# Optimization experiments

Measured on AMD Instinct MI355X. Metric: run time of the kernel, lower is better.

## Reference

```python
import jax, jax.numpy as jnp
import numpy as np

LEAK = 0.01  # torch LeakyReLU default negative_slope

def lrelu(x):
    return jnp.where(x >= 0, x, LEAK * x)

def edge_conv(x, src, dst, ea, W1, b1, W2, b2):
    # message: cat(x_i=target, x_j=source, edge_attr) -> Linear -> LeakyReLU -> Linear
    m = jnp.concatenate([x[dst], x[src], ea], axis=1)          # [E, 2F+Fe]
    h = lrelu(m @ W1 + b1) @ W2 + b2                            # [E, H]
    n = x.shape[0]
    agg = jnp.full((n, h.shape[1]), jnp.inf, h.dtype).at[dst].min(h)  # scatter-min at target
    return jnp.where(jnp.isfinite(agg), agg, jnp.zeros_like(agg))     # empty nodes -> 0


def setup_inputs() -> dict:
    key = jax.random.key(0)
    ks = jax.random.split(key, 20)
    B, N, E = 4, 20000, 640000
    NF, AD, EF, H = 2, 1, 1, 8
    inp = {
        "node_features": jax.random.randint(ks[0], (B, N, NF), 0, 10, dtype=jnp.int32),
        "actions": jax.random.normal(ks[1], (B, N), dtype=jnp.float32),
        "edge_index": jax.random.randint(ks[2], (B, 2, E), 0, N, dtype=jnp.int64),
        "edge_features": jax.random.normal(ks[3], (B, E, EF), dtype=jnp.float32),
    }
    d0 = NF + AD  # 3
    def lin(k, fin, fout):
        s = 1.0 / np.sqrt(fin)
        k1, k2 = jax.random.split(k)
        return (jax.random.uniform(k1, (fin, fout), jnp.float32, -s, s),
                jax.random.uniform(k2, (fout,), jnp.float32, -s, s))
    inp["c1_W1"], inp["c1_b1"] = lin(ks[4], 2 * d0 + EF, H)
    inp["c1_W2"], inp["c1_b2"] = lin(ks[5], H, H)
    inp["c2_W1"], inp["c2_b1"] = lin(ks[6], 2 * H + 1, H)
    inp["c2_W2"], inp["c2_b2"] = lin(ks[7], H, H)
    inp["c3_W1"], inp["c3_b1"] = lin(ks[8], 2 * H + 1, H)
    inp["c3_W2"], inp["c3_b2"] = lin(ks[9], H, H)
    inp["lin_W"], inp["lin_b"] = lin(ks[10], d0 + H, 1)
    return inp


def reference(node_features, actions, edge_index, edge_features,
              c1_W1, c1_b1, c1_W2, c1_b2,
              c2_W1, c2_b1, c2_W2, c2_b2,
              c3_W1, c3_b1, c3_W2, c3_b2,
              lin_W, lin_b):
    # x = int(node_features) concat actions  -> float
    x0 = jnp.concatenate([node_features.astype(jnp.int32).astype(jnp.float32),
                          actions[..., None]], axis=-1)  # [B,N,3]

    def per_graph(x0g, eig, eag):
        src, dst = eig[0], eig[1]  # flow source_to_target: x_j=src, x_i=dst
        h = lrelu(edge_conv(x0g, src, dst, eag, c1_W1, c1_b1, c1_W2, c1_b2))
        h = lrelu(edge_conv(h, src, dst, eag, c2_W1, c2_b1, c2_W2, c2_b2))
        h = lrelu(edge_conv(h, src, dst, eag, c3_W1, c3_b1, c3_W2, c3_b2))
        xc = jnp.concatenate([x0g, h], axis=1)  # [N, 3+8]
        return jnp.sum(xc, axis=0)              # sum-pool over nodes

    pooled = jax.vmap(per_graph)(x0, edge_index, edge_features)  # [B, 11]
    return pooled @ lin_W + lin_b  # [B, 1]
```

## Files before the change

### kernel.cpp

```cpp
#include <hip/hip_runtime.h>
#include <hip/hip_cooperative_groups.h>

namespace cg = cooperative_groups;

#define LEAK 0.01f
#define BS 128
#define PCHUNK 4096
#define PT 512
#define CT 512
#define MAXNB 256
#define CPGMAX 256

__device__ __forceinline__ float lrelu(float v) {
    return v >= 0.f ? v : LEAK * v;
}

__device__ __forceinline__ unsigned int fmin_encode(float x) {
    unsigned int u = __float_as_uint(x);
    return (u & 0x80000000u) ? ~u : (u | 0x80000000u);
}
__device__ __forceinline__ float fmin_decode(unsigned int k) {
    unsigned int u = (k & 0x80000000u) ? (k ^ 0x80000000u) : ~k;
    return __uint_as_float(u);
}

__device__ __forceinline__ unsigned int bf16_rne(float f) {
    unsigned int u = __float_as_uint(f);
    return (u + 0x7FFFu + ((u >> 16) & 1u)) >> 16;
}

__device__ __forceinline__ void block_add(float c, float* dst) {
    __shared__ float wsum[8];
#pragma unroll
    for (int off = 32; off > 0; off >>= 1) c += __shfl_down(c, off, 64);
    int lane = threadIdx.x & 63;
    int wave = threadIdx.x >> 6;
    if (lane == 0) wsum[wave] = c;
    __syncthreads();
    if (threadIdx.x == 0) {
        float s = 0.f;
        int nw = blockDim.x >> 6;
        for (int w = 0; w < nw; ++w) s += wsum[w];
        atomicAdd(dst, s);
    }
}


__device__ void init_body(
    const int* __restrict__ nf, const float* __restrict__ act,
    const float* __restrict__ W1, const float* __restrict__ b1,
    const float* __restrict__ lw, const float* __restrict__ lb,
    float* __restrict__ a1, unsigned short* __restrict__ a2,
    float* __restrict__ out, int N, int b, int ib) {
    int t = threadIdx.x;
    int n = ib * PT + t;
    float c = 0.f;
    if (n < N) {
        size_t i = (size_t)b * N + n;
        float x0 = (float)nf[i * 2 + 0];
        float x1 = (float)nf[i * 2 + 1];
        float x2 = act[i];
        float v1[8], v2[8];
#pragma unroll
        for (int j = 0; j < 8; ++j) {
            v1[j] = b1[j] + x0 * W1[0 * 8 + j] + x1 * W1[1 * 8 + j] + x2 * W1[2 * 8 + j];
            v2[j] =         x0 * W1[3 * 8 + j] + x1 * W1[4 * 8 + j] + x2 * W1[5 * 8 + j];
        }
        float4* o1 = (float4*)(a1 + i * 8);
        o1[0] = make_float4(v1[0], v1[1], v1[2], v1[3]);
        o1[1] = make_float4(v1[4], v1[5], v1[6], v1[7]);
        unsigned int w[4];
#pragma unroll
        for (int q = 0; q < 4; ++q)
            w[q] = bf16_rne(v2[2 * q]) | (bf16_rne(v2[2 * q + 1]) << 16);
        *(int4*)(a2 + i * 8) = make_int4(w[0], w[1], w[2], w[3]);
        c = x0 * lw[0] + x1 * lw[1] + x2 * lw[2];
        if (n == 0) c += lb[0];
    }
    block_add(c, &out[b]);
}

__device__ void part_body(
    const int* __restrict__ ei, const float* __restrict__ ea,
    int2* __restrict__ pairs, int* __restrict__ ofs,
    int E, int NB, int CPG, int b, int c,
    int* __restrict__ lc, int* __restrict__ lofs, int* __restrict__ ts) {
    int t = threadIdx.x;
    for (int i = t; i < NB; i += PT) lc[i] = 0;
    __syncthreads();

    int e0 = c * PCHUNK;
    int end = min(e0 + PCHUNK, E);
    const int* srow = ei + (size_t)b * 2 * E;
    const int* drow = srow + E;

    int pk[PCHUNK / PT];
#pragma unroll
    for (int j = 0; j < PCHUNK / PT; ++j) {
        int e = e0 + j * PT + t;
        int p = -1;
        if (e < end) {
            int d = drow[e];
            int bin = d >> 7;
            int r = atomicAdd(&lc[bin], 1);
            p = bin | ((d & 127) << 10) | (r << 17);
        }
        pk[j] = p;
    }
    __syncthreads();

    int v = (t < NB) ? lc[t] : 0;
    ts[t] = v;
    __syncthreads();
    int incl = v;
    for (int off = 1; off < PT; off <<= 1) {
        int add = (t >= off) ? ts[t - off] : 0;
        __syncthreads();
        incl += add;
        ts[t] = incl;
        __syncthreads();
    }
    if (t < NB) lofs[t] = incl - v;
    if (t == PT - 1) lofs[NB] = incl;
    __syncthreads();

    for (int i = t; i <= NB; i += PT) {
        int w = lofs[i];
        ofs[((size_t)b * (NB + 1) + i) * CPG + c] = w;
        if (i < NB) lc[i] = w;
    }
    __syncthreads();

    size_t pbase = (size_t)b * E + e0;
#pragma unroll
    for (int j = 0; j < PCHUNK / PT; ++j) {
        int e = e0 + j * PT + t;
        if (e < end) {
            int p = pk[j];
            int bin = p & 1023;
            int dl = (p >> 10) & 127;
            int r = p >> 17;
            int pos = lc[bin] + r;
            pairs[pbase + pos] =
                make_int2(srow[e] | (dl << 16), __float_as_int(ea[(size_t)b * E + e]));
        }
    }
}

__device__ __forceinline__ void conv_edge_compute(
    const float* we, const float* bb, const float* __restrict__ W2,
    int2 p, int4 raw, const float* __restrict__ a1s,
    unsigned int* __restrict__ acc) {
    int dl = (p.x >> 16) & 127;
    float eav = __int_as_float(p.y);
    unsigned int wq[4] = {(unsigned int)raw.x, (unsigned int)raw.y,
                          (unsigned int)raw.z, (unsigned int)raw.w};
    float a2v[8];
#pragma unroll
    for (int q = 0; q < 4; ++q) {
        a2v[2 * q]     = __uint_as_float(wq[q] << 16);
        a2v[2 * q + 1] = __uint_as_float(wq[q] & 0xFFFF0000u);
    }
    float h1[8];
#pragma unroll
    for (int j = 0; j < 8; ++j) {
        h1[j] = a1s[dl * 9 + j] + a2v[j];
        h1[j] = fmaf(eav, we[j], h1[j]);
        h1[j] = lrelu(h1[j]);
    }
    float h2[8];
#pragma unroll
    for (int j = 0; j < 8; ++j) h2[j] = bb[j];
#pragma unroll
    for (int kk = 0; kk < 8; ++kk) {
        float hk = h1[kk];
#pragma unroll
        for (int j = 0; j < 8; ++j) h2[j] = fmaf(hk, W2[kk * 8 + j], h2[j]);
    }
#pragma unroll
    for (int j = 0; j < 8; ++j)
        atomicMin(&acc[dl * 9 + j], fmin_encode(h2[j]));
}

__device__ void conv_edges_runs(
    const unsigned short* __restrict__ a2g, const float* we, const float* bb,
    const float* __restrict__ W2, const int2* __restrict__ pairsg,
    const int* __restrict__ ofb, int CPG,
    const float* __restrict__ a1s, unsigned int* __restrict__ acc,
    int* __restrict__ rs, int* __restrict__ re) {
    int t = threadIdx.x;
    for (int c = t; c < CPG; c += CT) {
        rs[c] = ofb[c];
        re[c] = ofb[CPG + c];
    }
    __syncthreads();
    int sw = t >> 5, sub = t & 31;
    const int nsw = CT >> 5;
    for (int c = sw; c < CPG; c += nsw) {
        int cb = c * PCHUNK;
        int k1 = cb + re[c];
        for (int k = cb + rs[c] + sub; k < k1; k += 32) {
            int2 p = pairsg[k];
            int4 v = *(const int4*)(a2g + (size_t)(p.x & 0xFFFF) * 8);
            conv_edge_compute(we, bb, W2, p, v, a1s, acc);
        }
    }
}

__device__ void conv_mid_body(
    const float* __restrict__ a1, const unsigned short* __restrict__ a2,
    const float* __restrict__ w1e, const float* __restrict__ W2,
    const float* __restrict__ b2,
    const float* __restrict__ nW1, const float* __restrict__ nb1,
    const int* __restrict__ ofs, const int2* __restrict__ pairs,
    float* __restrict__ na1, unsigned short* __restrict__ na2,
    int N, int NB, int CPG, int E, int b, int bin,
    float* __restrict__ a1s, unsigned int* __restrict__ acc,
    int* __restrict__ rs, int* __restrict__ re) {
    int n0 = bin << 7;
    int nCnt = min(BS, N - n0);
    int t = threadIdx.x;
    size_t node0 = (size_t)b * N + n0;

    for (int i = t; i < nCnt * 8; i += CT)
        a1s[(i >> 3) * 9 + (i & 7)] = a1[node0 * 8 + i];
    for (int i = t; i < BS * 9; i += CT) acc[i] = 0xFFFFFFFFu;
    float we[8], bb[8];
#pragma unroll
    for (int j = 0; j < 8; ++j) { we[j] = w1e[j]; bb[j] = b2[j]; }
    __syncthreads();

    conv_edges_runs(a2 + (size_t)b * N * 8, we, bb, W2,
                    pairs + (size_t)b * E,
                    ofs + ((size_t)b * (NB + 1) + bin) * CPG,
                    CPG, a1s, acc, rs, re);
    __syncthreads();

    for (int i = t; i < nCnt * 8; i += CT) {
        float v = fmin_decode(acc[(i >> 3) * 9 + (i & 7)]);
        unsigned int u = __float_as_uint(v);
        if ((u & 0x7F800000u) == 0x7F800000u) v = 0.f;
        a1s[(i >> 3) * 9 + (i & 7)] = lrelu(v);
    }
    __syncthreads();

    for (int nh = t; nh < nCnt * 2; nh += CT) {
        int node = nh >> 1, half = nh & 1;
        float h[8];
#pragma unroll
        for (int j = 0; j < 8; ++j) h[j] = a1s[node * 9 + j];
        float v[8];
#pragma unroll
        for (int j = 0; j < 8; ++j) v[j] = half ? 0.f : nb1[j];
        const float* Wbase = nW1 + (half ? 64 : 0);
#pragma unroll
        for (int k = 0; k < 8; ++k) {
            float hk = h[k];
#pragma unroll
            for (int j = 0; j < 8; ++j) v[j] = fmaf(hk, Wbase[k * 8 + j], v[j]);
        }
        if (half) {
            unsigned int w[4];
#pragma unroll
            for (int q = 0; q < 4; ++q)
                w[q] = bf16_rne(v[2 * q]) | (bf16_rne(v[2 * q + 1]) << 16);
            *(int4*)(na2 + (node0 + node) * 8) = make_int4(w[0], w[1], w[2], w[3]);
        } else {
            float4* o = (float4*)(na1 + (node0 + node) * 8);
            o[0] = make_float4(v[0], v[1], v[2], v[3]);
            o[1] = make_float4(v[4], v[5], v[6], v[7]);
        }
    }
    __syncthreads();
}

__device__ void conv_final_body(
    const float* __restrict__ a1, const unsigned short* __restrict__ a2,
    const float* __restrict__ w1e, const float* __restrict__ W2,
    const float* __restrict__ b2, const float* __restrict__ lw,
    const int* __restrict__ ofs, const int2* __restrict__ pairs,
    float* __restrict__ out, int N, int NB, int CPG, int E, int b, int bin,
    float* __restrict__ a1s, unsigned int* __restrict__ acc,
    int* __restrict__ rs, int* __restrict__ re) {
    int n0 = bin << 7;
    int nCnt = min(BS, N - n0);
    int t = threadIdx.x;
    size_t node0 = (size_t)b * N + n0;

    for (int i = t; i < nCnt * 8; i += CT)
        a1s[(i >> 3) * 9 + (i & 7)] = a1[node0 * 8 + i];
    for (int i = t; i < BS * 9; i += CT) acc[i] = 0xFFFFFFFFu;
    float we[8], bb[8];
#pragma unroll
    for (int j = 0; j < 8; ++j) { we[j] = w1e[j]; bb[j] = b2[j]; }
    __syncthreads();

    conv_edges_runs(a2 + (size_t)b * N * 8, we, bb, W2,
                    pairs + (size_t)b * E,
                    ofs + ((size_t)b * (NB + 1) + bin) * CPG,
                    CPG, a1s, acc, rs, re);
    __syncthreads();

    float c = 0.f;
    if (t < nCnt) {
#pragma unroll
        for (int j = 0; j < 8; ++j) {
            float v = fmin_decode(acc[t * 9 + j]);
            unsigned int u = __float_as_uint(v);
            if ((u & 0x7F800000u) == 0x7F800000u) v = 0.f;
            c = fmaf(lrelu(v), lw[3 + j], c);
        }
    }
    __syncthreads();
    block_add(c, &out[b]);
}


struct MegaParams {
    const int* ei; const float* ea;
    int2* pairs; int* ofs;
    const int* nf; const float* act;
    const float* W11; const float* b11; const float* W21; const float* b21;
    const float* W12; const float* b12; const float* W22; const float* b22;
    const float* W13; const float* b13; const float* W23; const float* b23;
    const float* lw; const float* lb;
    float* a1A; unsigned short* a2A; float* a1B; unsigned short* a2B;
    float* out;
    int E, N, NB, CPG, initBlocks;
};

__global__ __launch_bounds__(512, 8) void mega_kernel(MegaParams P) {
    cg::grid_group grid = cg::this_grid();
    __shared__ int lc[MAXNB];
    __shared__ int lofs[MAXNB + 1];
    __shared__ int ts[PT];
    __shared__ float a1s[BS * 9];
    __shared__ unsigned int acc[BS * 9];
    __shared__ int rs[CPGMAX];
    __shared__ int re[CPGMAX];
    int b = blockIdx.y, bx = blockIdx.x;

    if (bx < P.CPG)
        part_body(P.ei, P.ea, P.pairs, P.ofs, P.E, P.NB, P.CPG, b, bx, lc, lofs, ts);
    else if (bx - P.CPG < P.initBlocks)
        init_body(P.nf, P.act, P.W11, P.b11, P.lw, P.lb, P.a1A, P.a2A, P.out,
                  P.N, b, bx - P.CPG);
    __threadfence();
    grid.sync();
    if (bx < P.NB)
        conv_mid_body(P.a1A, P.a2A, P.W11 + 6 * 8, P.W21, P.b21, P.W12, P.b12,
                      P.ofs, P.pairs, P.a1B, P.a2B, P.N, P.NB, P.CPG, P.E,
                      b, bx, a1s, acc, rs, re);
    __threadfence();
    grid.sync();
    if (bx < P.NB)
        conv_mid_body(P.a1B, P.a2B, P.W12 + 16 * 8, P.W22, P.b22, P.W13, P.b13,
                      P.ofs, P.pairs, P.a1A, P.a2A, P.N, P.NB, P.CPG, P.E,
                      b, bx, a1s, acc, rs, re);
    __threadfence();
    grid.sync();
    if (bx < P.NB)
        conv_final_body(P.a1A, P.a2A, P.W13 + 16 * 8, P.W23, P.b23, P.lw,
                        P.ofs, P.pairs, P.out, P.N, P.NB, P.CPG, P.E,
                        b, bx, a1s, acc, rs, re);
}


__global__ __launch_bounds__(PT) void part_init_kernel(
    const int* __restrict__ ei, const float* __restrict__ ea,
    int2* __restrict__ pairs, int* __restrict__ ofs,
    const int* __restrict__ nf, const float* __restrict__ act,
    const float* __restrict__ W1, const float* __restrict__ b1,
    const float* __restrict__ lw, const float* __restrict__ lb,
    float* __restrict__ a1, unsigned short* __restrict__ a2,
    float* __restrict__ out, int E, int N, int NB, int CPG) {
    __shared__ int lc[MAXNB];
    __shared__ int lofs[MAXNB + 1];
    __shared__ int ts[PT];
    int b = blockIdx.y;
    if (blockIdx.x >= CPG) {
        init_body(nf, act, W1, b1, lw, lb, a1, a2, out, N, b, blockIdx.x - CPG);
        return;
    }
    part_body(ei, ea, pairs, ofs, E, NB, CPG, b, blockIdx.x, lc, lofs, ts);
}

__global__ __launch_bounds__(CT) void conv_mid_kernel(
    const float* __restrict__ a1, const unsigned short* __restrict__ a2,
    const float* __restrict__ w1e, const float* __restrict__ W2,
    const float* __restrict__ b2,
    const float* __restrict__ nW1, const float* __restrict__ nb1,
    const int* __restrict__ ofs, const int2* __restrict__ pairs,
    float* __restrict__ na1, unsigned short* __restrict__ na2,
    int N, int NB, int CPG, int E) {
    __shared__ float a1s[BS * 9];
    __shared__ unsigned int acc[BS * 9];
    __shared__ int rs[CPGMAX];
    __shared__ int re[CPGMAX];
    conv_mid_body(a1, a2, w1e, W2, b2, nW1, nb1, ofs, pairs, na1, na2,
                  N, NB, CPG, E, blockIdx.y, blockIdx.x, a1s, acc, rs, re);
}

__global__ __launch_bounds__(CT) void conv_final_kernel(
    const float* __restrict__ a1, const unsigned short* __restrict__ a2,
    const float* __restrict__ w1e, const float* __restrict__ W2,
    const float* __restrict__ b2, const float* __restrict__ lw,
    const int* __restrict__ ofs, const int2* __restrict__ pairs,
    float* __restrict__ out, int N, int NB, int CPG, int E) {
    __shared__ float a1s[BS * 9];
    __shared__ unsigned int acc[BS * 9];
    __shared__ int rs[CPGMAX];
    __shared__ int re[CPGMAX];
    conv_final_body(a1, a2, w1e, W2, b2, lw, ofs, pairs, out,
                    N, NB, CPG, E, blockIdx.y, blockIdx.x, a1s, acc, rs, re);
}


__global__ __launch_bounds__(256) void node_init_kernel(
    const int* __restrict__ nf, const float* __restrict__ act,
    float* __restrict__ x0, int BN) {
    int tid = blockIdx.x * blockDim.x + threadIdx.x;
    if (tid >= BN) return;
    x0[tid * 3 + 0] = (float)nf[tid * 2 + 0];
    x0[tid * 3 + 1] = (float)nf[tid * 2 + 1];
    x0[tid * 3 + 2] = act[tid];
}

template <int D>
__global__ __launch_bounds__(256) void edge_conv_kernel(
    const float* __restrict__ x, const int* __restrict__ ei,
    const float* __restrict__ ea,
    const float* __restrict__ W1, const float* __restrict__ b1,
    const float* __restrict__ W2, const float* __restrict__ b2,
    unsigned int* __restrict__ agg, int E, int N, int B) {
    int tid = blockIdx.x * blockDim.x + threadIdx.x;
    if (tid >= B * E) return;
    int b = tid / E;
    int e = tid - b * E;
    const int* eb = ei + (size_t)b * 2 * E;
    int s = eb[e];
    int d = eb[E + e];
    const float* xi = x + ((size_t)b * N + d) * D;
    const float* xj = x + ((size_t)b * N + s) * D;
    constexpr int M = 2 * D + 1;
    float m[M];
#pragma unroll
    for (int k = 0; k < D; ++k) { m[k] = xi[k]; m[D + k] = xj[k]; }
    m[2 * D] = ea[(size_t)b * E + e];
    float h1[8];
#pragma unroll
    for (int j = 0; j < 8; ++j) h1[j] = b1[j];
#pragma unroll
    for (int k = 0; k < M; ++k) {
        float mk = m[k];
#pragma unroll
        for (int j = 0; j < 8; ++j) h1[j] = fmaf(mk, W1[k * 8 + j], h1[j]);
    }
#pragma unroll
    for (int j = 0; j < 8; ++j) h1[j] = lrelu(h1[j]);
    float h2[8];
#pragma unroll
    for (int j = 0; j < 8; ++j) h2[j] = b2[j];
#pragma unroll
    for (int k = 0; k < 8; ++k) {
        float hk = h1[k];
#pragma unroll
        for (int j = 0; j < 8; ++j) h2[j] = fmaf(hk, W2[k * 8 + j], h2[j]);
    }
    unsigned int* ag = agg + ((size_t)b * N + d) * 8;
#pragma unroll
    for (int j = 0; j < 8; ++j) atomicMin(&ag[j], fmin_encode(h2[j]));
}

__global__ __launch_bounds__(256) void finalize_kernel(
    unsigned int* __restrict__ agg, int total) {
    int tid = blockIdx.x * blockDim.x + threadIdx.x;
    if (tid >= total) return;
    float v = fmin_decode(agg[tid]);
    unsigned int u = __float_as_uint(v);
    if ((u & 0x7F800000u) == 0x7F800000u) v = 0.f;
    ((float*)agg)[tid] = lrelu(v);
}

__global__ __launch_bounds__(256) void pool_kernel(
    const float* __restrict__ x0, const float* __restrict__ h,
    const float* __restrict__ lw, const float* __restrict__ lb,
    float* __restrict__ out, int N) {
    int b = blockIdx.y;
    int n = blockIdx.x * blockDim.x + threadIdx.x;
    float c = 0.f;
    if (n < N) {
        const float* x = x0 + ((size_t)b * N + n) * 3;
        const float* hh = h + ((size_t)b * N + n) * 8;
        c = x[0] * lw[0] + x[1] * lw[1] + x[2] * lw[2];
#pragma unroll
        for (int k = 0; k < 8; ++k) c = fmaf(hh[k], lw[3 + k], c);
        if (n == 0) c += lb[0];
    }
    block_add(c, &out[b]);
}


static inline size_t align256(size_t x) { return (x + 255) & ~(size_t)255; }

extern "C" void kernel_launch(void* const* d_in, const int* in_sizes, int n_in,
                              void* d_out, int out_size, void* d_ws, size_t ws_size,
                              hipStream_t stream) {
    const int B = 4;
    const int N = in_sizes[1] / B;
    const int E = in_sizes[2] / (2 * B);

    const int*   nf  = (const int*)d_in[0];
    const float* act = (const float*)d_in[1];
    const int*   ei  = (const int*)d_in[2];
    const float* ea  = (const float*)d_in[3];
    const float* c1_W1 = (const float*)d_in[4];
    const float* c1_b1 = (const float*)d_in[5];
    const float* c1_W2 = (const float*)d_in[6];
    const float* c1_b2 = (const float*)d_in[7];
    const float* c2_W1 = (const float*)d_in[8];
    const float* c2_b1 = (const float*)d_in[9];
    const float* c2_W2 = (const float*)d_in[10];
    const float* c2_b2 = (const float*)d_in[11];
    const float* c3_W1 = (const float*)d_in[12];
    const float* c3_b1 = (const float*)d_in[13];
    const float* c3_W2 = (const float*)d_in[14];
    const float* c3_b2 = (const float*)d_in[15];
    const float* lw    = (const float*)d_in[16];
    const float* lb    = (const float*)d_in[17];
    float* out = (float*)d_out;

    const int BN = B * N;
    const int BE = B * E;
    const int NB = (N + BS - 1) / BS;
    const int CPG = (E + PCHUNK - 1) / PCHUNK;
    const int initBlocks = (N + PT - 1) / PT;

    char* ws = (char*)d_ws;
    size_t off = 0;
    float* a1A = (float*)(ws + off);           off += align256((size_t)BN * 8 * 4);
    float* a1B = (float*)(ws + off);           off += align256((size_t)BN * 8 * 4);
    unsigned short* a2A = (unsigned short*)(ws + off); off += align256((size_t)BN * 8 * 2);
    unsigned short* a2B = (unsigned short*)(ws + off); off += align256((size_t)BN * 8 * 2);
    int* ofs    = (int*)(ws + off);    off += align256((size_t)B * (NB + 1) * CPG * 4);
    int2* pairs = (int2*)(ws + off);   off += align256((size_t)BE * 8);
    float* x0   = (float*)(ws + off);  off += align256((size_t)BN * 3 * 4);
    const bool useFast = (off <= ws_size) && (NB <= MAXNB) && (CPG <= CPGMAX) &&
                         (N <= 32768);

    hipMemsetAsync(out, 0, (size_t)B * sizeof(float), stream);

    if (useFast) {
        const int gx = (CPG + initBlocks > NB) ? (CPG + initBlocks) : NB;

        int dev = 0;
        hipGetDevice(&dev);
        int numCU = 0;
        hipDeviceGetAttribute(&numCU, hipDeviceAttributeMultiprocessorCount, dev);
        int occ = 0;
        hipOccupancyMaxActiveBlocksPerMultiprocessor(&occ, mega_kernel, 512, 0);
        const bool canCoop = (occ > 0) && ((size_t)occ * (size_t)numCU >=
                                           (size_t)gx * (size_t)B);

        if (canCoop) {
            MegaParams P;
            P.ei = ei; P.ea = ea; P.pairs = pairs; P.ofs = ofs;
            P.nf = nf; P.act = act;
            P.W11 = c1_W1; P.b11 = c1_b1; P.W21 = c1_W2; P.b21 = c1_b2;
            P.W12 = c2_W1; P.b12 = c2_b1; P.W22 = c2_W2; P.b22 = c2_b2;
            P.W13 = c3_W1; P.b13 = c3_b1; P.W23 = c3_W2; P.b23 = c3_b2;
            P.lw = lw; P.lb = lb;
            P.a1A = a1A; P.a2A = a2A; P.a1B = a1B; P.a2B = a2B;
            P.out = out;
            P.E = E; P.N = N; P.NB = NB; P.CPG = CPG; P.initBlocks = initBlocks;
            void* args[] = {&P};
            hipLaunchCooperativeKernel((void*)mega_kernel, dim3(gx, B),
                                       dim3(512), args, 0, stream);
        } else {
            dim3 pgrid(CPG + initBlocks, B);
            dim3 cgrid(NB, B);
            part_init_kernel<<<pgrid, PT, 0, stream>>>(
                ei, ea, pairs, ofs, nf, act, c1_W1, c1_b1, lw, lb,
                a1A, a2A, out, E, N, NB, CPG);
            conv_mid_kernel<<<cgrid, CT, 0, stream>>>(
                a1A, a2A, c1_W1 + 6 * 8, c1_W2, c1_b2, c2_W1, c2_b1,
                ofs, pairs, a1B, a2B, N, NB, CPG, E);
            conv_mid_kernel<<<cgrid, CT, 0, stream>>>(
                a1B, a2B, c2_W1 + 16 * 8, c2_W2, c2_b2, c3_W1, c3_b1,
                ofs, pairs, a1A, a2A, N, NB, CPG, E);
            conv_final_kernel<<<cgrid, CT, 0, stream>>>(
                a1A, a2A, c3_W1 + 16 * 8, c3_W2, c3_b2, lw,
                ofs, pairs, out, N, NB, CPG, E);
        }
    } else {
        const int egrid = (BE + 255) / 256;
        const int aggTotal = BN * 8;
        const int agrid = (aggTotal + 255) / 256;
        const size_t aggBytes = (size_t)aggTotal * 4;
        unsigned int* uA = (unsigned int*)a1A;
        unsigned int* uB = (unsigned int*)a1B;

        node_init_kernel<<<(BN + 255) / 256, 256, 0, stream>>>(nf, act, x0, BN);

        hipMemsetAsync(uA, 0xFF, aggBytes, stream);
        edge_conv_kernel<3><<<egrid, 256, 0, stream>>>(
            x0, ei, ea, c1_W1, c1_b1, c1_W2, c1_b2, uA, E, N, B);
        finalize_kernel<<<agrid, 256, 0, stream>>>(uA, aggTotal);

        hipMemsetAsync(uB, 0xFF, aggBytes, stream);
        edge_conv_kernel<8><<<egrid, 256, 0, stream>>>(
            (const float*)uA, ei, ea, c2_W1, c2_b1, c2_W2, c2_b2, uB, E, N, B);
        finalize_kernel<<<agrid, 256, 0, stream>>>(uB, aggTotal);

        hipMemsetAsync(uA, 0xFF, aggBytes, stream);
        edge_conv_kernel<8><<<egrid, 256, 0, stream>>>(
            (const float*)uB, ei, ea, c3_W1, c3_b1, c3_W2, c3_b2, uA, E, N, B);
        finalize_kernel<<<agrid, 256, 0, stream>>>(uA, aggTotal);

        dim3 plgrid((N + 255) / 256, B);
        pool_kernel<<<plgrid, 256, 0, stream>>>(x0, (const float*)uA, lw, lb, out, N);
    }
}
```

Before: 208.7 us.

## Add per-bin sort by destination node to replace shared atomicMin with register reductions

Adds a sort stage after partitioning that counts edges per bin globally, builds per-destination-node histograms, and scatters edge pairs into a fully destination-sorted array. The three conv stages then give each 32-lane group one destination node, keep running minima in registers and reduce with shuffles, which removes the eight shared-memory atomicMin operations per edge and the float-encoding step. The cost is an extra pass over all edges with a grid-wide sync, a second edge buffer, and load imbalance when node degrees vary.

```diff
diff --git a/kernel.cpp b/kernel.cpp
--- a/kernel.cpp
+++ b/kernel.cpp
@@ -7,7 +7,6 @@
 #define BS 128
 #define PCHUNK 4096
 #define PT 512
-#define CT 512
 #define MAXNB 256
 #define CPGMAX 256
 
@@ -82,7 +81,7 @@
 
 __device__ void part_body(
     const int* __restrict__ ei, const float* __restrict__ ea,
-    int2* __restrict__ pairs, int* __restrict__ ofs,
+    int2* __restrict__ pairs, int* __restrict__ ofs, int* __restrict__ bcnt,
     int E, int NB, int CPG, int b, int c,
     int* __restrict__ lc, int* __restrict__ lofs, int* __restrict__ ts) {
     int t = threadIdx.x;
@@ -110,6 +109,7 @@
     __syncthreads();
 
     int v = (t < NB) ? lc[t] : 0;
+    if (t < NB && v) atomicAdd(&bcnt[b * NB + t], v);
     ts[t] = v;
     __syncthreads();
     int incl = v;
@@ -147,62 +147,131 @@
     }
 }
 
-__device__ __forceinline__ void conv_edge_compute(
-    const float* we, const float* bb, const float* __restrict__ W2,
-    int2 p, int4 raw, const float* __restrict__ a1s,
-    unsigned int* __restrict__ acc) {
-    int dl = (p.x >> 16) & 127;
-    float eav = __int_as_float(p.y);
-    unsigned int wq[4] = {(unsigned int)raw.x, (unsigned int)raw.y,
-                          (unsigned int)raw.z, (unsigned int)raw.w};
-    float a2v[8];
-#pragma unroll
-    for (int q = 0; q < 4; ++q) {
-        a2v[2 * q]     = __uint_as_float(wq[q] << 16);
-        a2v[2 * q + 1] = __uint_as_float(wq[q] & 0xFFFF0000u);
-    }
-    float h1[8];
-#pragma unroll
-    for (int j = 0; j < 8; ++j) {
-        h1[j] = a1s[dl * 9 + j] + a2v[j];
-        h1[j] = fmaf(eav, we[j], h1[j]);
-        h1[j] = lrelu(h1[j]);
-    }
-    float h2[8];
-#pragma unroll
-    for (int j = 0; j < 8; ++j) h2[j] = bb[j];
-#pragma unroll
-    for (int kk = 0; kk < 8; ++kk) {
-        float hk = h1[kk];
-#pragma unroll
-        for (int j = 0; j < 8; ++j) h2[j] = fmaf(hk, W2[kk * 8 + j], h2[j]);
-    }
-#pragma unroll
-    for (int j = 0; j < 8; ++j)
-        atomicMin(&acc[dl * 9 + j], fmin_encode(h2[j]));
-}
-
-__device__ void conv_edges_runs(
-    const unsigned short* __restrict__ a2g, const float* we, const float* bb,
-    const float* __restrict__ W2, const int2* __restrict__ pairsg,
-    const int* __restrict__ ofb, int CPG,
-    const float* __restrict__ a1s, unsigned int* __restrict__ acc,
-    int* __restrict__ rs, int* __restrict__ re) {
+__device__ void sort_body(
+    const int* __restrict__ ofs_bbin, const int* __restrict__ bcnt_b,
+    const int2* __restrict__ pairsg, int2* __restrict__ spairsg,
+    int* __restrict__ segofs_b, int* __restrict__ dlofs_bbin,
+    int NB, int CPG, int bin,
+    int* __restrict__ rs, int* __restrict__ re,
+    int* __restrict__ hist, int* __restrict__ cursor, int* __restrict__ red) {
     int t = threadIdx.x;
-    for (int c = t; c < CPG; c += CT) {
-        rs[c] = ofb[c];
-        re[c] = ofb[CPG + c];
-    }
-    __syncthreads();
+    for (int c = t; c < CPG; c += PT) {
+        rs[c] = ofs_bbin[c];
+        re[c] = ofs_bbin[CPG + c];
+    }
+    for (int i = t; i < BS; i += PT) hist[i] = 0;
+
+    int part = 0;
+    for (int i = t; i < bin; i += PT) part += bcnt_b[i];
+#pragma unroll
+    for (int off = 32; off > 0; off >>= 1) part += __shfl_down(part, off, 64);
+    if ((t & 63) == 0) red[t >> 6] = part;
+    __syncthreads();
+    if (t == 0) {
+        int s = 0;
+        for (int w = 0; w < PT / 64; ++w) s += red[w];
+        red[0] = s;
+    }
+    __syncthreads();
+    int seg0 = red[0];
+    int cnt = bcnt_b[bin];
+    if (t == 0) {
+        segofs_b[bin] = seg0;
+        if (bin == NB - 1) segofs_b[NB] = seg0 + cnt;
+    }
+
     int sw = t >> 5, sub = t & 31;
-    const int nsw = CT >> 5;
+    const int nsw = PT >> 5;
+    for (int c = sw; c < CPG; c += nsw) {
+        int cb = c * PCHUNK;
+        int k1 = cb + re[c];
+        for (int k = cb + rs[c] + sub; k < k1; k += 32)
+            atomicAdd(&hist[(pairsg[k].x >> 16) & 127], 1);
+    }
+    __syncthreads();
+
+    if (t < BS) cursor[t] = hist[t];
+    __syncthreads();
+    for (int off = 1; off < BS; off <<= 1) {
+        int add = 0;
+        if (t < BS && t >= off) add = cursor[t - off];
+        __syncthreads();
+        if (t < BS) cursor[t] += add;
+        __syncthreads();
+    }
+    if (t < BS) cursor[t] -= hist[t];
+    __syncthreads();
+
+    if (t < BS) dlofs_bbin[t] = cursor[t];
+    if (t == 0) dlofs_bbin[BS] = cnt;
+    __syncthreads();
+
     for (int c = sw; c < CPG; c += nsw) {
         int cb = c * PCHUNK;
         int k1 = cb + re[c];
         for (int k = cb + rs[c] + sub; k < k1; k += 32) {
             int2 p = pairsg[k];
-            int4 v = *(const int4*)(a2g + (size_t)(p.x & 0xFFFF) * 8);
-            conv_edge_compute(we, bb, W2, p, v, a1s, acc);
+            int pos = atomicAdd(&cursor[(p.x >> 16) & 127], 1);
+            spairsg[seg0 + pos] = p;
+        }
+    }
+}
+
+__device__ void conv_core_sorted(
+    const unsigned short* __restrict__ a2g, const float* we, const float* bb,
+    const float* __restrict__ W2, const int2* __restrict__ spairsg,
+    int seg0, const int* __restrict__ dlofs,
+    const float* __restrict__ a1s, float* __restrict__ hres) {
+    int t = threadIdx.x;
+    int sw = t >> 5, sub = t & 31;
+    const int nsw = PT >> 5;
+    for (int dl = sw; dl < BS; dl += nsw) {
+        int g0 = seg0 + dlofs[dl];
+        int g1 = seg0 + dlofs[dl + 1];
+        float a1r[8];
+#pragma unroll
+        for (int j = 0; j < 8; ++j) a1r[j] = a1s[dl * 9 + j];
+        float m[8];
+#pragma unroll
+        for (int j = 0; j < 8; ++j) m[j] = __builtin_inff();
+        for (int k = g0 + sub; k < g1; k += 32) {
+            int2 p = spairsg[k];
+            float eav = __int_as_float(p.y);
+            int4 raw = *(const int4*)(a2g + (size_t)(p.x & 0xFFFF) * 8);
+            unsigned int wq[4] = {(unsigned int)raw.x, (unsigned int)raw.y,
+                                  (unsigned int)raw.z, (unsigned int)raw.w};
+            float h1[8];
+#pragma unroll
+            for (int q = 0; q < 4; ++q) {
+                h1[2 * q]     = a1r[2 * q]     + __uint_as_float(wq[q] << 16);
+                h1[2 * q + 1] = a1r[2 * q + 1] + __uint_as_float(wq[q] & 0xFFFF0000u);
+            }
+#pragma unroll
+            for (int j = 0; j < 8; ++j) {
+                h1[j] = fmaf(eav, we[j], h1[j]);
+                h1[j] = lrelu(h1[j]);
+            }
+            float h2[8];
+#pragma unroll
+            for (int j = 0; j < 8; ++j) h2[j] = bb[j];
+#pragma unroll
+            for (int kk = 0; kk < 8; ++kk) {
+                float hk = h1[kk];
+#pragma unroll
+                for (int j = 0; j < 8; ++j) h2[j] = fmaf(hk, W2[kk * 8 + j], h2[j]);
+            }
+#pragma unroll
+            for (int j = 0; j < 8; ++j) m[j] = fminf(m[j], h2[j]);
+        }
+#pragma unroll
+        for (int off = 16; off > 0; off >>= 1) {
+#pragma unroll
+            for (int j = 0; j < 8; ++j)
+                m[j] = fminf(m[j], __shfl_down(m[j], off, 32));
+        }
+        if (sub == 0) {
+#pragma unroll
+            for (int j = 0; j < 8; ++j) hres[dl * 9 + j] = m[j];
         }
     }
 }
@@ -212,39 +281,39 @@
     const float* __restrict__ w1e, const float* __restrict__ W2,
     const float* __restrict__ b2,
     const float* __restrict__ nW1, const float* __restrict__ nb1,
-    const int* __restrict__ ofs, const int2* __restrict__ pairs,
+    const int* __restrict__ segofs, const int* __restrict__ dlofs_g,
+    const int2* __restrict__ spairs,
     float* __restrict__ na1, unsigned short* __restrict__ na2,
-    int N, int NB, int CPG, int E, int b, int bin,
-    float* __restrict__ a1s, unsigned int* __restrict__ acc,
-    int* __restrict__ rs, int* __restrict__ re) {
+    int N, int NB, int E, int b, int bin,
+    float* __restrict__ a1s, float* __restrict__ hres, int* __restrict__ dlo) {
     int n0 = bin << 7;
     int nCnt = min(BS, N - n0);
     int t = threadIdx.x;
     size_t node0 = (size_t)b * N + n0;
 
-    for (int i = t; i < nCnt * 8; i += CT)
+    for (int i = t; i < nCnt * 8; i += PT)
         a1s[(i >> 3) * 9 + (i & 7)] = a1[node0 * 8 + i];
-    for (int i = t; i < BS * 9; i += CT) acc[i] = 0xFFFFFFFFu;
+    const int* dsrc = dlofs_g + ((size_t)b * NB + bin) * (BS + 1);
+    for (int i = t; i <= BS; i += PT) dlo[i] = dsrc[i];
     float we[8], bb[8];
 #pragma unroll
     for (int j = 0; j < 8; ++j) { we[j] = w1e[j]; bb[j] = b2[j]; }
-    __syncthreads();
-
-    conv_edges_runs(a2 + (size_t)b * N * 8, we, bb, W2,
-                    pairs + (size_t)b * E,
-                    ofs + ((size_t)b * (NB + 1) + bin) * CPG,
-                    CPG, a1s, acc, rs, re);
-    __syncthreads();
-
-    for (int i = t; i < nCnt * 8; i += CT) {
-        float v = fmin_decode(acc[(i >> 3) * 9 + (i & 7)]);
+    int seg0 = segofs[(size_t)b * (NB + 1) + bin];
+    __syncthreads();
+
+    conv_core_sorted(a2 + (size_t)b * N * 8, we, bb, W2,
+                     spairs + (size_t)b * E, seg0, dlo, a1s, hres);
+    __syncthreads();
+
+    for (int i = t; i < nCnt * 8; i += PT) {
+        float v = hres[(i >> 3) * 9 + (i & 7)];
         unsigned int u = __float_as_uint(v);
         if ((u & 0x7F800000u) == 0x7F800000u) v = 0.f;
         a1s[(i >> 3) * 9 + (i & 7)] = lrelu(v);
     }
     __syncthreads();
 
-    for (int nh = t; nh < nCnt * 2; nh += CT) {
+    for (int nh = t; nh < nCnt * 2; nh += PT) {
         int node = nh >> 1, half = nh & 1;
         float h[8];
 #pragma unroll
@@ -278,34 +347,34 @@
     const float* __restrict__ a1, const unsigned short* __restrict__ a2,
     const float* __restrict__ w1e, const float* __restrict__ W2,
     const float* __restrict__ b2, const float* __restrict__ lw,
-    const int* __restrict__ ofs, const int2* __restrict__ pairs,
-    float* __restrict__ out, int N, int NB, int CPG, int E, int b, int bin,
-    float* __restrict__ a1s, unsigned int* __restrict__ acc,
-    int* __restrict__ rs, int* __restrict__ re) {
+    const int* __restrict__ segofs, const int* __restrict__ dlofs_g,
+    const int2* __restrict__ spairs,
+    float* __restrict__ out, int N, int NB, int E, int b, int bin,
+    float* __restrict__ a1s, float* __restrict__ hres, int* __restrict__ dlo) {
     int n0 = bin << 7;
     int nCnt = min(BS, N - n0);
     int t = threadIdx.x;
     size_t node0 = (size_t)b * N + n0;
 
-    for (int i = t; i < nCnt * 8; i += CT)
+    for (int i = t; i < nCnt * 8; i += PT)
         a1s[(i >> 3) * 9 + (i & 7)] = a1[node0 * 8 + i];
-    for (int i = t; i < BS * 9; i += CT) acc[i] = 0xFFFFFFFFu;
+    const int* dsrc = dlofs_g + ((size_t)b * NB + bin) * (BS + 1);
+    for (int i = t; i <= BS; i += PT) dlo[i] = dsrc[i];
     float we[8], bb[8];
 #pragma unroll
     for (int j = 0; j < 8; ++j) { we[j] = w1e[j]; bb[j] = b2[j]; }
-    __syncthreads();
-
-    conv_edges_runs(a2 + (size_t)b * N * 8, we, bb, W2,
-                    pairs + (size_t)b * E,
-                    ofs + ((size_t)b * (NB + 1) + bin) * CPG,
-                    CPG, a1s, acc, rs, re);
+    int seg0 = segofs[(size_t)b * (NB + 1) + bin];
+    __syncthreads();
+
+    conv_core_sorted(a2 + (size_t)b * N * 8, we, bb, W2,
+                     spairs + (size_t)b * E, seg0, dlo, a1s, hres);
     __syncthreads();
 
     float c = 0.f;
     if (t < nCnt) {
 #pragma unroll
         for (int j = 0; j < 8; ++j) {
-            float v = fmin_decode(acc[t * 9 + j]);
+            float v = hres[t * 9 + j];
             unsigned int u = __float_as_uint(v);
             if ((u & 0x7F800000u) == 0x7F800000u) v = 0.f;
             c = fmaf(lrelu(v), lw[3 + j], c);
@@ -318,7 +387,7 @@
 
 struct MegaParams {
     const int* ei; const float* ea;
-    int2* pairs; int* ofs;
+    int2* pairs; int2* spairs; int* ofs; int* bcnt; int* segofs; int* dlofs;
     const int* nf; const float* act;
     const float* W11; const float* b11; const float* W21; const float* b21;
     const float* W12; const float* b12; const float* W22; const float* b22;
@@ -335,40 +404,52 @@
     __shared__ int lofs[MAXNB + 1];
     __shared__ int ts[PT];
     __shared__ float a1s[BS * 9];
-    __shared__ unsigned int acc[BS * 9];
-    __shared__ int rs[CPGMAX];
-    __shared__ int re[CPGMAX];
+    __shared__ float hres[BS * 9];
+    __shared__ int dlo[BS + 1];
+    __shared__ int hist[BS];
+    __shared__ int cursor[BS];
+    __shared__ int red[PT / 64];
     int b = blockIdx.y, bx = blockIdx.x;
 
     if (bx < P.CPG)
-        part_body(P.ei, P.ea, P.pairs, P.ofs, P.E, P.NB, P.CPG, b, bx, lc, lofs, ts);
+        part_body(P.ei, P.ea, P.pairs, P.ofs, P.bcnt, P.E, P.NB, P.CPG, b, bx,
+                  lc, lofs, ts);
     else if (bx - P.CPG < P.initBlocks)
         init_body(P.nf, P.act, P.W11, P.b11, P.lw, P.lb, P.a1A, P.a2A, P.out,
                   P.N, b, bx - P.CPG);
     __threadfence();
     grid.sync();
     if (bx < P.NB)
+        sort_body(P.ofs + ((size_t)b * (P.NB + 1) + bx) * P.CPG,
+                  P.bcnt + (size_t)b * P.NB,
+                  P.pairs + (size_t)b * P.E, P.spairs + (size_t)b * P.E,
+                  P.segofs + (size_t)b * (P.NB + 1),
+                  P.dlofs + ((size_t)b * P.NB + bx) * (BS + 1),
+                  P.NB, P.CPG, bx, lc, lofs, hist, cursor, red);
+    __threadfence();
+    grid.sync();
+    if (bx < P.NB)
         conv_mid_body(P.a1A, P.a2A, P.W11 + 6 * 8, P.W21, P.b21, P.W12, P.b12,
-                      P.ofs, P.pairs, P.a1B, P.a2B, P.N, P.NB, P.CPG, P.E,
-                      b, bx, a1s, acc, rs, re);
+                      P.segofs, P.dlofs, P.spairs, P.a1B, P.a2B,
+                      P.N, P.NB, P.E, b, bx, a1s, hres, dlo);
     __threadfence();
     grid.sync();
     if (bx < P.NB)
         conv_mid_body(P.a1B, P.a2B, P.W12 + 16 * 8, P.W22, P.b22, P.W13, P.b13,
-                      P.ofs, P.pairs, P.a1A, P.a2A, P.N, P.NB, P.CPG, P.E,
-                      b, bx, a1s, acc, rs, re);
+                      P.segofs, P.dlofs, P.spairs, P.a1A, P.a2A,
+                      P.N, P.NB, P.E, b, bx, a1s, hres, dlo);
     __threadfence();
     grid.sync();
     if (bx < P.NB)
         conv_final_body(P.a1A, P.a2A, P.W13 + 16 * 8, P.W23, P.b23, P.lw,
-                        P.ofs, P.pairs, P.out, P.N, P.NB, P.CPG, P.E,
-                        b, bx, a1s, acc, rs, re);
+                        P.segofs, P.dlofs, P.spairs, P.out,
+                        P.N, P.NB, P.E, b, bx, a1s, hres, dlo);
 }
 
 
 __global__ __launch_bounds__(PT) void part_init_kernel(
     const int* __restrict__ ei, const float* __restrict__ ea,
-    int2* __restrict__ pairs, int* __restrict__ ofs,
+    int2* __restrict__ pairs, int* __restrict__ ofs, int* __restrict__ bcnt,
     const int* __restrict__ nf, const float* __restrict__ act,
     const float* __restrict__ W1, const float* __restrict__ b1,
     const float* __restrict__ lw, const float* __restrict__ lb,
@@ -382,37 +463,55 @@
         init_body(nf, act, W1, b1, lw, lb, a1, a2, out, N, b, blockIdx.x - CPG);
         return;
     }
-    part_body(ei, ea, pairs, ofs, E, NB, CPG, b, blockIdx.x, lc, lofs, ts);
-}
-
-__global__ __launch_bounds__(CT) void conv_mid_kernel(
+    part_body(ei, ea, pairs, ofs, bcnt, E, NB, CPG, b, blockIdx.x, lc, lofs, ts);
+}
+
+__global__ __launch_bounds__(PT) void sort_kernel(
+    const int* __restrict__ ofs, const int* __restrict__ bcnt,
+    const int2* __restrict__ pairs, int2* __restrict__ spairs,
+    int* __restrict__ segofs, int* __restrict__ dlofs,
+    int NB, int CPG, int E) {
+    __shared__ int rs[CPGMAX];
+    __shared__ int re[CPGMAX];
+    __shared__ int hist[BS];
+    __shared__ int cursor[BS];
+    __shared__ int red[PT / 64];
+    int b = blockIdx.y, bin = blockIdx.x;
+    sort_body(ofs + ((size_t)b * (NB + 1) + bin) * CPG, bcnt + (size_t)b * NB,
+              pairs + (size_t)b * E, spairs + (size_t)b * E,
+              segofs + (size_t)b * (NB + 1),
+              dlofs + ((size_t)b * NB + bin) * (BS + 1),
+              NB, CPG, bin, rs, re, hist, cursor, red);
+}
+
+__global__ __launch_bounds__(PT) void conv_mid_kernel(
     const float* __restrict__ a1, const unsigned short* __restrict__ a2,
     const float* __restrict__ w1e, const float* __restrict__ W2,
     const float* __restrict__ b2,
     const float* __restrict__ nW1, const float* __restrict__ nb1,
-    const int* __restrict__ ofs, const int2* __restrict__ pairs,
+    const int* __restrict__ segofs, const int* __restrict__ dlofs,
+    const int2* __restrict__ spairs,
     float* __restrict__ na1, unsigned short* __restrict__ na2,
-    int N, int NB, int CPG, int E) {
+    int N, int NB, int E) {
     __shared__ float a1s[BS * 9];
-    __shared__ unsigned int acc[BS * 9];
-    __shared__ int rs[CPGMAX];
-    __shared__ int re[CPGMAX];
-    conv_mid_body(a1, a2, w1e, W2, b2, nW1, nb1, ofs, pairs, na1, na2,
-                  N, NB, CPG, E, blockIdx.y, blockIdx.x, a1s, acc, rs, re);
-}
-
-__global__ __launch_bounds__(CT) void conv_final_kernel(
+    __shared__ float hres[BS * 9];
+    __shared__ int dlo[BS + 1];
+    conv_mid_body(a1, a2, w1e, W2, b2, nW1, nb1, segofs, dlofs, spairs,
+                  na1, na2, N, NB, E, blockIdx.y, blockIdx.x, a1s, hres, dlo);
+}
+
+__global__ __launch_bounds__(PT) void conv_final_kernel(
     const float* __restrict__ a1, const unsigned short* __restrict__ a2,
     const float* __restrict__ w1e, const float* __restrict__ W2,
     const float* __restrict__ b2, const float* __restrict__ lw,
-    const int* __restrict__ ofs, const int2* __restrict__ pairs,
-    float* __restrict__ out, int N, int NB, int CPG, int E) {
+    const int* __restrict__ segofs, const int* __restrict__ dlofs,
+    const int2* __restrict__ spairs,
+    float* __restrict__ out, int N, int NB, int E) {
     __shared__ float a1s[BS * 9];
-    __shared__ unsigned int acc[BS * 9];
-    __shared__ int rs[CPGMAX];
-    __shared__ int re[CPGMAX];
-    conv_final_body(a1, a2, w1e, W2, b2, lw, ofs, pairs, out,
-                    N, NB, CPG, E, blockIdx.y, blockIdx.x, a1s, acc, rs, re);
+    __shared__ float hres[BS * 9];
+    __shared__ int dlo[BS + 1];
+    conv_final_body(a1, a2, w1e, W2, b2, lw, segofs, dlofs, spairs, out,
+                    N, NB, E, blockIdx.y, blockIdx.x, a1s, hres, dlo);
 }
 
 
@@ -543,7 +642,11 @@
     unsigned short* a2A = (unsigned short*)(ws + off); off += align256((size_t)BN * 8 * 2);
     unsigned short* a2B = (unsigned short*)(ws + off); off += align256((size_t)BN * 8 * 2);
     int* ofs    = (int*)(ws + off);    off += align256((size_t)B * (NB + 1) * CPG * 4);
+    int* bcnt   = (int*)(ws + off);    off += align256((size_t)B * NB * 4);
+    int* segofs = (int*)(ws + off);    off += align256((size_t)B * (NB + 1) * 4);
+    int* dlofs  = (int*)(ws + off);    off += align256((size_t)B * NB * (BS + 1) * 4);
     int2* pairs = (int2*)(ws + off);   off += align256((size_t)BE * 8);
+    int2* spairs = (int2*)(ws + off);  off += align256((size_t)BE * 8);
     float* x0   = (float*)(ws + off);  off += align256((size_t)BN * 3 * 4);
     const bool useFast = (off <= ws_size) && (NB <= MAXNB) && (CPG <= CPGMAX) &&
                          (N <= 32768);
@@ -551,6 +654,7 @@
     hipMemsetAsync(out, 0, (size_t)B * sizeof(float), stream);
 
     if (useFast) {
+        hipMemsetAsync(bcnt, 0, (size_t)B * NB * 4, stream);
         const int gx = (CPG + initBlocks > NB) ? (CPG + initBlocks) : NB;
 
         int dev = 0;
@@ -558,13 +662,14 @@
         int numCU = 0;
         hipDeviceGetAttribute(&numCU, hipDeviceAttributeMultiprocessorCount, dev);
         int occ = 0;
-        hipOccupancyMaxActiveBlocksPerMultiprocessor(&occ, mega_kernel, 512, 0);
+        hipOccupancyMaxActiveBlocksPerMultiprocessor(&occ, mega_kernel, PT, 0);
         const bool canCoop = (occ > 0) && ((size_t)occ * (size_t)numCU >=
                                            (size_t)gx * (size_t)B);
 
         if (canCoop) {
             MegaParams P;
-            P.ei = ei; P.ea = ea; P.pairs = pairs; P.ofs = ofs;
+            P.ei = ei; P.ea = ea; P.pairs = pairs; P.spairs = spairs;
+            P.ofs = ofs; P.bcnt = bcnt; P.segofs = segofs; P.dlofs = dlofs;
             P.nf = nf; P.act = act;
             P.W11 = c1_W1; P.b11 = c1_b1; P.W21 = c1_W2; P.b21 = c1_b2;
             P.W12 = c2_W1; P.b12 = c2_b1; P.W22 = c2_W2; P.b22 = c2_b2;
@@ -575,22 +680,24 @@
             P.E = E; P.N = N; P.NB = NB; P.CPG = CPG; P.initBlocks = initBlocks;
             void* args[] = {&P};
             hipLaunchCooperativeKernel((void*)mega_kernel, dim3(gx, B),
-                                       dim3(512), args, 0, stream);
+                                       dim3(PT), args, 0, stream);
         } else {
             dim3 pgrid(CPG + initBlocks, B);
             dim3 cgrid(NB, B);
             part_init_kernel<<<pgrid, PT, 0, stream>>>(
-                ei, ea, pairs, ofs, nf, act, c1_W1, c1_b1, lw, lb,
+                ei, ea, pairs, ofs, bcnt, nf, act, c1_W1, c1_b1, lw, lb,
                 a1A, a2A, out, E, N, NB, CPG);
-            conv_mid_kernel<<<cgrid, CT, 0, stream>>>(
+            sort_kernel<<<cgrid, PT, 0, stream>>>(ofs, bcnt, pairs, spairs,
+                                                  segofs, dlofs, NB, CPG, E);
+            conv_mid_kernel<<<cgrid, PT, 0, stream>>>(
                 a1A, a2A, c1_W1 + 6 * 8, c1_W2, c1_b2, c2_W1, c2_b1,
-                ofs, pairs, a1B, a2B, N, NB, CPG, E);
-            conv_mid_kernel<<<cgrid, CT, 0, stream>>>(
+                segofs, dlofs, spairs, a1B, a2B, N, NB, E);
+            conv_mid_kernel<<<cgrid, PT, 0, stream>>>(
                 a1B, a2B, c2_W1 + 16 * 8, c2_W2, c2_b2, c3_W1, c3_b1,
-                ofs, pairs, a1A, a2A, N, NB, CPG, E);
-            conv_final_kernel<<<cgrid, CT, 0, stream>>>(
+                segofs, dlofs, spairs, a1A, a2A, N, NB, E);
+            conv_final_kernel<<<cgrid, PT, 0, stream>>>(
                 a1A, a2A, c3_W1 + 16 * 8, c3_W2, c3_b2, lw,
-                ofs, pairs, out, N, NB, CPG, E);
+                segofs, dlofs, spairs, out, N, NB, E);
         }
     } else {
         const int egrid = (BE + 255) / 256;
```

New measurement: 328.7 us. +57.5%, slower.
